# Optimization experiments

Measured on AMD Instinct MI355X. Metric: run time of the kernel, lower is better.

The kernel has to match this reference:

```python
import jax, jax.numpy as jnp
import numpy as np

VOCAB_SIZE = 4096
D_EMBED = 256
BETA = 0.25  # unused: module returns raw commit_loss; beta applied by caller


def setup_inputs() -> dict:
    key = jax.random.key(0)
    k_h, k_e = jax.random.split(key)
    h = jax.random.normal(k_h, (16, D_EMBED, 32, 32), dtype=jnp.float32)
    embedding = jax.random.normal(k_e, (VOCAB_SIZE, D_EMBED), dtype=jnp.float32)
    return {"h": h, "embedding": embedding}


def reference(h, embedding):
    B, C, H, W = h.shape
    h = h.astype(jnp.float32)
    # (B, C, H, W) -> (N, C) with N = B*H*W
    h_flat = jnp.transpose(h, (0, 2, 3, 1)).reshape(-1, C)
    dist = (
        jnp.sum(h_flat * h_flat, axis=1, keepdims=True)
        + jnp.sum(embedding * embedding, axis=1)
        - 2.0 * jnp.einsum("nc,vc->nv", h_flat, embedding)
    )
    indices_flat = jnp.argmin(dist, axis=1)
    indices = indices_flat.reshape(B, H, W)
    # gather codebook vectors and restore (B, C, H, W)
    z_q = jnp.transpose(embedding[indices_flat].reshape(B, H, W, C), (0, 3, 1, 2))
    commit_loss = jnp.mean((h - jax.lax.stop_gradient(z_q)) ** 2)
    # straight-through estimator
    z_q_st = h + jax.lax.stop_gradient(z_q - h)
    return z_q_st, indices, commit_loss
```

## Files before the change

### kernel.cpp

```cpp
#include <hip/hip_runtime.h>

#define D 256
#define VOCAB 4096
#define NTOT 16384
#define N_OUT0 4194304

typedef _Float16 half8 __attribute__((ext_vector_type(8)));
typedef float f32x4 __attribute__((ext_vector_type(4)));
typedef unsigned long long u64;

__device__ __forceinline__ u64 pack_key(float d, int v) {
    unsigned u = __float_as_uint(d);
    u ^= ((unsigned)((int)u >> 31)) | 0x80000000u;
    return ((u64)u << 32) | (unsigned)v;
}

__device__ __forceinline__ float unpack_dist(u64 k) {
    unsigned u = (unsigned)(k >> 32);
    u = (u & 0x80000000u) ? (u ^ 0x80000000u) : ~u;
    return __uint_as_float(u);
}

__global__ __launch_bounds__(256) void k_pack(const float* __restrict__ h,
                                              const float* __restrict__ emb,
                                              _Float16* __restrict__ Apk,
                                              _Float16* __restrict__ Bpk,
                                              float* __restrict__ hsqp,
                                              float* __restrict__ ht,
                                              float* __restrict__ esq,
                                              float* __restrict__ e2maxp,
                                              float* __restrict__ out2) {
    __shared__ float S[8192];
    const int tid = threadIdx.x;
    const int bid = blockIdx.x;
    if (bid < 512) {
        const int bm = bid >> 3, w = bid & 7;
        const int b = bm >> 2, p0 = (bm & 3) * 256;
        const float* src = h + ((size_t)b << 18) + p0;
#pragma unroll 4
        for (int cl = 0; cl < 32; ++cl)
            S[cl * 256 + tid] = src[(size_t)(w * 32 + cl) << 10 | (unsigned)tid];
        __syncthreads();
        float sq = 0.0f;
#pragma unroll
        for (int cl = 0; cl < 32; ++cl) {
            float t = S[cl * 256 + tid];
            sq = fmaf(t, t, sq);
        }
        hsqp[(size_t)(bm * 8 + w) * 256 + tid] = sq;
        float* htr = ht + ((size_t)(bm * 256 + tid)) * D + w * 32;
#pragma unroll
        for (int c4 = 0; c4 < 8; ++c4) {
            float4 t;
            t.x = S[(c4 * 4 + 0) * 256 + tid];
            t.y = S[(c4 * 4 + 1) * 256 + tid];
            t.z = S[(c4 * 4 + 2) * 256 + tid];
            t.w = S[(c4 * 4 + 3) * 256 + tid];
            *(float4*)(htr + c4 * 4) = t;
        }
        _Float16* dstT = Apk + (size_t)bm * 65536 + (size_t)w * 8192;
#pragma unroll
        for (int i = 0; i < 4; ++i) {
            alignas(16) _Float16 hi[8];
#pragma unroll
            for (int j = 0; j < 8; ++j) hi[j] = (_Float16)S[(i * 8 + j) * 256 + tid];
            *(half8*)(dstT + i * 2048 + tid * 8) = *(half8*)hi;
        }
    } else if (bid < 768) {
        const int bid2 = bid - 512;
        const int bn = bid2 >> 3, w = bid2 & 7;
        const int v0 = bn * 128;
#pragma unroll 4
        for (int i = 0; i < 16; ++i) {
            int flat = i * 256 + tid;
            int r = flat >> 5, cl = flat & 31;
            S[cl * 129 + r] = emb[(size_t)(v0 + r) * D + w * 32 + cl];
        }
        __syncthreads();
        _Float16* dstT = Bpk + (size_t)bn * 32768 + (size_t)w * 4096;
#pragma unroll
        for (int i = 0; i < 2; ++i) {
            int s = i * 256 + tid;
            int q = s >> 7, r = s & 127;
            alignas(16) _Float16 hi[8];
#pragma unroll
            for (int j = 0; j < 8; ++j) hi[j] = (_Float16)S[(q * 8 + j) * 129 + r];
            *(half8*)(dstT + q * 1024 + r * 8) = *(half8*)hi;
        }
    } else {
        __shared__ float sm[4];
        const int pid = bid - 768;
        const int lane = tid & 63, wv = tid >> 6;
        const int v0 = pid * 64;
        float lmax = 0.0f;
#pragma unroll 4
        for (int i = 0; i < 16; ++i) {
            int v = v0 + i * 4 + wv;
            float4 e = *(const float4*)(emb + (size_t)v * D + lane * 4);
            float s = e.x * e.x + e.y * e.y + e.z * e.z + e.w * e.w;
#pragma unroll
            for (int m = 32; m >= 1; m >>= 1) s += __shfl_xor(s, m, 64);
            if (lane == 0) esq[v] = s;
            lmax = fmaxf(lmax, s);
        }
        if (lane == 0) sm[wv] = lmax;
        __syncthreads();
        if (tid == 0) {
            e2maxp[pid] = fmaxf(fmaxf(sm[0], sm[1]), fmaxf(sm[2], sm[3]));
            if (pid == 0) out2[0] = 0.0f;
        }
    }
}

__global__ __launch_bounds__(256, 3) void k_gemm(const _Float16* __restrict__ Apk,
                                                 const _Float16* __restrict__ Bpk,
                                                 const float* __restrict__ esq,
                                                 u64* __restrict__ keys2) {
    __shared__ u64 t2[4096];

    const int tid = threadIdx.x;
    const int bid = blockIdx.x;
    const int swz = (bid & 7) * 512 + (bid >> 3);
    const int bm = swz >> 5, bn = swz & 31;
    const int m0 = bm * 128, n0 = bn * 128;

    const int wv = tid >> 6, l = tid & 63;
    const int wm = wv & 1, wn = wv >> 1;
    const int quad = l >> 4, j16 = l & 15;

    const _Float16* aP = Apk + (size_t)(bm >> 1) * 65536 + (size_t)(bm & 1) * 1024
                       + quad * 2048 + (wm * 64 + j16) * 8;
    const _Float16* bP = Bpk + (size_t)bn * 32768
                       + quad * 1024 + (wn * 64 + j16) * 8;

    f32x4 acc[4][4];
#pragma unroll
    for (int i = 0; i < 4; ++i)
#pragma unroll
        for (int j = 0; j < 4; ++j) acc[i][j] = (f32x4)0.0f;

    half8 af[4], bf[4], afn[4], bfn[4];
#pragma unroll
    for (int mt = 0; mt < 4; ++mt) af[mt] = *(const half8*)(aP + mt * 128);
#pragma unroll
    for (int nt = 0; nt < 4; ++nt) bf[nt] = *(const half8*)(bP + nt * 128);

#pragma unroll
    for (int w = 0; w < 8; ++w) {
        if (w < 7) {
#pragma unroll
            for (int mt = 0; mt < 4; ++mt)
                afn[mt] = *(const half8*)(aP + (w + 1) * 8192 + mt * 128);
#pragma unroll
            for (int nt = 0; nt < 4; ++nt)
                bfn[nt] = *(const half8*)(bP + (w + 1) * 4096 + nt * 128);
        }
        __builtin_amdgcn_s_setprio(1);
#pragma unroll
        for (int mt = 0; mt < 4; ++mt)
#pragma unroll
            for (int nt = 0; nt < 4; ++nt)
                acc[mt][nt] = __builtin_amdgcn_mfma_f32_16x16x32_f16(af[mt], bf[nt], acc[mt][nt], 0, 0, 0);
        __builtin_amdgcn_s_setprio(0);
#pragma unroll
        for (int mt = 0; mt < 4; ++mt) af[mt] = afn[mt];
#pragma unroll
        for (int nt = 0; nt < 4; ++nt) bf[nt] = bfn[nt];
    }

    float es[4];
    int vidx[4];
#pragma unroll
    for (int nt = 0; nt < 4; ++nt) {
        vidx[nt] = n0 + wn * 64 + nt * 16 + j16;
        es[nt] = esq[vidx[nt]];
    }

    u64 M1 = ~0ULL, M2 = ~0ULL;
#pragma unroll
    for (int pass = 0; pass < 2; ++pass) {
        if (wn == pass) {
#pragma unroll
            for (int mt = 0; mt < 4; ++mt) {
#pragma unroll
                for (int r = 0; r < 4; ++r) {
                    float d1 = __builtin_inff(), d2 = __builtin_inff();
                    int i1 = 0, i2 = 0;
#pragma unroll
                    for (int nt = 0; nt < 4; ++nt) {
                        float dv = es[nt] - 2.0f * acc[mt][nt][r];
                        bool c1 = dv < d1;
                        bool c2 = dv < d2;
                        d2 = c1 ? d1 : (c2 ? dv : d2);
                        i2 = c1 ? i1 : (c2 ? vidx[nt] : i2);
                        d1 = c1 ? dv : d1;
                        i1 = c1 ? vidx[nt] : i1;
                    }
                    int row = wm * 64 + mt * 16 + quad * 4 + r;
                    u64* p = t2 + ((size_t)(row * 16 + (j16 ^ (row & 7))) * 2);
                    p[0] = pack_key(d1, i1);
                    p[1] = pack_key(d2, i2);
                }
            }
        }
        __syncthreads();
        if (tid < 128) {
            const int row = tid;
#pragma unroll
            for (int j = 0; j < 16; ++j) {
                const u64* p = t2 + ((size_t)(row * 16 + (j ^ (row & 7))) * 2);
                u64 a1 = p[0], a2 = p[1];
                u64 x = M1 > a1 ? M1 : a1;
                M1 = M1 < a1 ? M1 : a1;
                u64 y = M2 < a2 ? M2 : a2;
                M2 = x < y ? x : y;
            }
        }
        __syncthreads();
    }
    if (tid < 128) {
        keys2[(size_t)(m0 + tid) * 64 + bn * 2 + 0] = M1;
        keys2[(size_t)(m0 + tid) * 64 + bn * 2 + 1] = M2;
    }
}

__device__ __forceinline__ u64 exact_key_ht(const float* __restrict__ ht,
                                            const float* __restrict__ emb,
                                            const float* __restrict__ esq,
                                            int rg, int v, int lane) {
    const float4 h4 = *(const float4*)(ht + (size_t)rg * D + lane * 4);
    const float4 e4 = *(const float4*)(emb + (size_t)v * D + lane * 4);
    float p = h4.x * e4.x;
    p = fmaf(h4.y, e4.y, p);
    p = fmaf(h4.z, e4.z, p);
    p = fmaf(h4.w, e4.w, p);
#pragma unroll
    for (int m = 32; m >= 1; m >>= 1) p += __shfl_xor(p, m, 64);
    return pack_key(esq[v] - 2.0f * p, v);
}

__global__ __launch_bounds__(256) void k_refine(const float* __restrict__ ht,
                                                const float* __restrict__ emb,
                                                const float* __restrict__ esq,
                                                const float* __restrict__ hsqp,
                                                const float* __restrict__ e2maxp,
                                                const u64* __restrict__ keys2,
                                                float* __restrict__ out1) {
    __shared__ float sE2;
    const int tid = threadIdx.x;
    const int lane = tid & 63;
    const int w = tid >> 6;
    const int n0 = blockIdx.x * 32;

    if (tid < 64) {
        float m = e2maxp[tid];
#pragma unroll
        for (int s = 32; s >= 1; s >>= 1) m = fmaxf(m, __shfl_xor(m, s, 64));
        if (tid == 0) sE2 = m;
    }
    __syncthreads();
    const float e2m = sE2;

    int rg = n0 + w * 8;
    u64 key = keys2[(size_t)rg * 64 + lane];
#pragma unroll 1
    for (int rr = 0; rr < 8; ++rr, ++rg) {
        u64 keyn = 0;
        if (rr < 7) keyn = keys2[(size_t)(rg + 1) * 64 + lane];
        u64 gm = key;
#pragma unroll
        for (int m = 32; m >= 1; m >>= 1) {
            u64 o = __shfl_xor(gm, m, 64);
            gm = o < gm ? o : gm;
        }
        float hq = 0.0f;
#pragma unroll
        for (int k = 0; k < 8; ++k) hq += hsqp[(size_t)(rg >> 8) * 2048 + k * 256 + (rg & 255)];
        const float thr = unpack_dist(gm) + 4.0e-3f * sqrtf(hq * e2m) + 1e-2f;
        u64 cmask = __ballot(unpack_dist(key) <= thr);
        u64 bestk;
        if (__popcll(cmask) == 1) {
            bestk = gm;
        } else {
            bestk = ~0ULL;
            u64 rescan = 0;
            u64 cm = cmask;
            while (cm) {
                int L = __ffsll((long long)cm) - 1;
                cm &= cm - 1;
                if (L & 1) {
                    rescan |= 1ull << (L >> 1);
                } else {
                    u64 kL = __shfl(key, L, 64);
                    u64 ek = exact_key_ht(ht, emb, esq, rg, (int)(kL & 0xFFFFFFFFu), lane);
                    bestk = ek < bestk ? ek : bestk;
                }
            }
            while (rescan) {
                int bnr = __ffsll((long long)rescan) - 1;
                rescan &= rescan - 1;
                const float* htr = ht + (size_t)rg * D;
                u64 k0 = ~0ULL, k1 = ~0ULL;
#pragma unroll
                for (int c = 0; c < 2; ++c) {
                    int v = bnr * 128 + c * 64 + lane;
                    float p = 0.0f;
#pragma unroll 8
                    for (int d = 0; d < D; d += 4) {
                        float4 hh = *(const float4*)(htr + d);
                        float4 ee = *(const float4*)(emb + (size_t)v * D + d);
                        p = fmaf(hh.x, ee.x, p);
                        p = fmaf(hh.y, ee.y, p);
                        p = fmaf(hh.z, ee.z, p);
                        p = fmaf(hh.w, ee.w, p);
                    }
                    u64 kc = pack_key(esq[v] - 2.0f * p, v);
                    if (c == 0) k0 = kc; else k1 = kc;
                }
                u64 m1 = k0 < k1 ? k0 : k1, m2 = k0 < k1 ? k1 : k0;
#pragma unroll
                for (int m = 32; m >= 1; m >>= 1) {
                    u64 o1 = __shfl_xor(m1, m, 64), o2 = __shfl_xor(m2, m, 64);
                    u64 hi = m1 > o1 ? m1 : o1;
                    m1 = m1 < o1 ? m1 : o1;
                    u64 lo2 = m2 < o2 ? m2 : o2;
                    m2 = hi < lo2 ? hi : lo2;
                }
                u64 e1 = exact_key_ht(ht, emb, esq, rg, (int)(m1 & 0xFFFFFFFFu), lane);
                u64 e2 = exact_key_ht(ht, emb, esq, rg, (int)(m2 & 0xFFFFFFFFu), lane);
                bestk = e1 < bestk ? e1 : bestk;
                bestk = e2 < bestk ? e2 : bestk;
            }
        }
        if (lane == 0) out1[rg] = (float)(int)(bestk & 0xFFFFFFFFu);
        key = keyn;
    }
}

__global__ __launch_bounds__(256) void k_out(const float* __restrict__ h,
                                             const float* __restrict__ emb,
                                             const float* __restrict__ out1,
                                             float* __restrict__ out0,
                                             float* __restrict__ out2) {
    __shared__ float zq[32][260];
    __shared__ float wred[4];
    const int tid = threadIdx.x;
    const int lane = tid & 63;
    const int w = tid >> 6;
    const int n0 = blockIdx.x * 32;
    const int b = n0 >> 10;
    const int p0 = n0 & 1023;
#pragma unroll
    for (int rr = 0; rr < 8; ++rr) {
        int r = w * 8 + rr;
        unsigned idx = (unsigned)(int)out1[n0 + r];
        float4 e4 = *(const float4*)(emb + (size_t)idx * D + lane * 4);
        *(float4*)&zq[r][lane * 4] = e4;
    }
    __syncthreads();
    float lsum = 0.0f;
    const size_t base = ((size_t)b * D) << 10;
#pragma unroll 4
    for (int it = 0; it < 32; ++it) {
        int c = it * 8 + (tid >> 5);
        int pp = tid & 31;
        float z = zq[pp][c];
        size_t g = base + ((size_t)c << 10) + p0 + pp;
        float hv = h[g];
        out0[g] = hv + (z - hv);
        float d = hv - z;
        lsum = fmaf(d, d, lsum);
    }
#pragma unroll
    for (int m = 32; m >= 1; m >>= 1) lsum += __shfl_xor(lsum, m, 64);
    if (lane == 0) wred[w] = lsum;
    __syncthreads();
    if (tid == 0)
        atomicAdd(out2, (wred[0] + wred[1] + wred[2] + wred[3]) * (1.0f / (float)N_OUT0));
}

extern "C" void kernel_launch(void* const* d_in, const int* in_sizes, int n_in,
                              void* d_out, int out_size, void* d_ws, size_t ws_size,
                              hipStream_t stream) {
    const float* h = (const float*)d_in[0];
    const float* emb = (const float*)d_in[1];
    float* out0 = (float*)d_out;
    float* out1 = out0 + N_OUT0;
    float* out2 = out1 + NTOT;

    char* wsb = (char*)d_ws;
    _Float16* Apk = (_Float16*)wsb;
    _Float16* Bpk = (_Float16*)(wsb + 8388608);
    float* esq = (float*)(wsb + 10485760);
    float* hsqp = (float*)(wsb + 10502144);
    float* e2maxp = (float*)(wsb + 11026432);
    u64* keys2 = (u64*)(wsb + 11028480);

    hipLaunchKernelGGL(k_pack, dim3(832), dim3(256), 0, stream, h, emb, Apk, Bpk, hsqp, out0, esq, e2maxp, out2);
    hipLaunchKernelGGL(k_gemm, dim3(4096), dim3(256), 0, stream, Apk, Bpk, esq, keys2);
    hipLaunchKernelGGL(k_refine, dim3(NTOT / 32), dim3(256), 0, stream, out0, emb, esq, hsqp, e2maxp, keys2, out1);
    hipLaunchKernelGGL(k_out, dim3(NTOT / 32), dim3(256), 0, stream, h, emb, out1, out0, out2);
}
```

Before: 181.3 us.

## Pack codebook index into float low mantissa bits for top-2 candidate keys

Replaces 64-bit (distance,index) keys in the GEMM epilogue with 32-bit floats whose low 7 mantissa bits carry the local codebook index. The top-2 selection then uses fminf/fmaxf instead of 64-bit compares and selects, and the LDS scratch and global key buffer shrink by half. The refine kernel recovers full indices from the lane position plus the embedded bits. Because this truncates distance precision, the candidate threshold is widened (1e-2 to 5e-2) to keep the exact rescoring correct, which may send more rows down the slower rescan path.

```diff
diff --git a/kernel.cpp b/kernel.cpp
--- a/kernel.cpp
+++ b/kernel.cpp
@@ -13,12 +13,6 @@
     unsigned u = __float_as_uint(d);
     u ^= ((unsigned)((int)u >> 31)) | 0x80000000u;
     return ((u64)u << 32) | (unsigned)v;
-}
-
-__device__ __forceinline__ float unpack_dist(u64 k) {
-    unsigned u = (unsigned)(k >> 32);
-    u = (u & 0x80000000u) ? (u ^ 0x80000000u) : ~u;
-    return __uint_as_float(u);
 }
 
 __global__ __launch_bounds__(256) void k_pack(const float* __restrict__ h,
@@ -115,8 +109,8 @@
 __global__ __launch_bounds__(256, 3) void k_gemm(const _Float16* __restrict__ Apk,
                                                  const _Float16* __restrict__ Bpk,
                                                  const float* __restrict__ esq,
-                                                 u64* __restrict__ keys2) {
-    __shared__ u64 t2[4096];
+                                                 float2* __restrict__ keys2) {
+    __shared__ float2 t2[2048];
 
     const int tid = threadIdx.x;
     const int bid = blockIdx.x;
@@ -169,14 +163,14 @@
     }
 
     float es[4];
-    int vidx[4];
+    unsigned code[4];
 #pragma unroll
     for (int nt = 0; nt < 4; ++nt) {
-        vidx[nt] = n0 + wn * 64 + nt * 16 + j16;
-        es[nt] = esq[vidx[nt]];
-    }
-
-    u64 M1 = ~0ULL, M2 = ~0ULL;
+        code[nt] = (unsigned)(wn * 64 + nt * 16 + j16);
+        es[nt] = esq[n0 + (int)code[nt]];
+    }
+
+    float M1 = __builtin_inff(), M2 = __builtin_inff();
 #pragma unroll
     for (int pass = 0; pass < 2; ++pass) {
         if (wn == pass) {
@@ -184,22 +178,18 @@
             for (int mt = 0; mt < 4; ++mt) {
 #pragma unroll
                 for (int r = 0; r < 4; ++r) {
-                    float d1 = __builtin_inff(), d2 = __builtin_inff();
-                    int i1 = 0, i2 = 0;
+                    float c[4];
 #pragma unroll
                     for (int nt = 0; nt < 4; ++nt) {
                         float dv = es[nt] - 2.0f * acc[mt][nt][r];
-                        bool c1 = dv < d1;
-                        bool c2 = dv < d2;
-                        d2 = c1 ? d1 : (c2 ? dv : d2);
-                        i2 = c1 ? i1 : (c2 ? vidx[nt] : i2);
-                        d1 = c1 ? dv : d1;
-                        i1 = c1 ? vidx[nt] : i1;
+                        c[nt] = __uint_as_float((__float_as_uint(dv) & ~127u) | code[nt]);
                     }
+                    float p = fminf(c[0], c[1]), q = fmaxf(c[0], c[1]);
+                    float rr = fminf(c[2], c[3]), s = fmaxf(c[2], c[3]);
+                    float m1 = fminf(p, rr);
+                    float m2 = fminf(fmaxf(p, rr), fminf(q, s));
                     int row = wm * 64 + mt * 16 + quad * 4 + r;
-                    u64* p = t2 + ((size_t)(row * 16 + (j16 ^ (row & 7))) * 2);
-                    p[0] = pack_key(d1, i1);
-                    p[1] = pack_key(d2, i2);
+                    t2[row * 16 + (j16 ^ (row & 7))] = make_float2(m1, m2);
                 }
             }
         }
@@ -208,20 +198,16 @@
             const int row = tid;
 #pragma unroll
             for (int j = 0; j < 16; ++j) {
-                const u64* p = t2 + ((size_t)(row * 16 + (j ^ (row & 7))) * 2);
-                u64 a1 = p[0], a2 = p[1];
-                u64 x = M1 > a1 ? M1 : a1;
-                M1 = M1 < a1 ? M1 : a1;
-                u64 y = M2 < a2 ? M2 : a2;
-                M2 = x < y ? x : y;
+                float2 a = t2[row * 16 + (j ^ (row & 7))];
+                float t = fmaxf(M1, a.x);
+                M1 = fminf(M1, a.x);
+                M2 = fminf(fminf(M2, a.y), t);
             }
         }
         __syncthreads();
     }
-    if (tid < 128) {
-        keys2[(size_t)(m0 + tid) * 64 + bn * 2 + 0] = M1;
-        keys2[(size_t)(m0 + tid) * 64 + bn * 2 + 1] = M2;
-    }
+    if (tid < 128)
+        keys2[(size_t)(m0 + tid) * 32 + bn] = make_float2(M1, M2);
 }
 
 __device__ __forceinline__ u64 exact_key_ht(const float* __restrict__ ht,
@@ -244,7 +230,7 @@
                                                 const float* __restrict__ esq,
                                                 const float* __restrict__ hsqp,
                                                 const float* __restrict__ e2maxp,
-                                                const u64* __restrict__ keys2,
+                                                const float* __restrict__ keys2f,
                                                 float* __restrict__ out1) {
     __shared__ float sE2;
     const int tid = threadIdx.x;
@@ -262,27 +248,26 @@
     const float e2m = sE2;
 
     int rg = n0 + w * 8;
-    u64 key = keys2[(size_t)rg * 64 + lane];
+    float key = keys2f[(size_t)rg * 64 + lane];
 #pragma unroll 1
     for (int rr = 0; rr < 8; ++rr, ++rg) {
-        u64 keyn = 0;
-        if (rr < 7) keyn = keys2[(size_t)(rg + 1) * 64 + lane];
-        u64 gm = key;
-#pragma unroll
-        for (int m = 32; m >= 1; m >>= 1) {
-            u64 o = __shfl_xor(gm, m, 64);
-            gm = o < gm ? o : gm;
-        }
+        float keyn = 0.0f;
+        if (rr < 7) keyn = keys2f[(size_t)(rg + 1) * 64 + lane];
+        float gm = key;
+#pragma unroll
+        for (int m = 32; m >= 1; m >>= 1) gm = fminf(gm, __shfl_xor(gm, m, 64));
         float hq = 0.0f;
 #pragma unroll
         for (int k = 0; k < 8; ++k) hq += hsqp[(size_t)(rg >> 8) * 2048 + k * 256 + (rg & 255)];
-        const float thr = unpack_dist(gm) + 4.0e-3f * sqrtf(hq * e2m) + 1e-2f;
-        u64 cmask = __ballot(unpack_dist(key) <= thr);
-        u64 bestk;
+        const float thr = gm + 4.0e-3f * sqrtf(hq * e2m) + 5.0e-2f;
+        u64 cmask = __ballot(key <= thr);
+        int bidx;
         if (__popcll(cmask) == 1) {
-            bestk = gm;
+            u64 own = __ballot(key == gm);
+            int L = __ffsll((long long)own) - 1;
+            bidx = (L >> 1) * 128 + (int)(__float_as_uint(gm) & 127u);
         } else {
-            bestk = ~0ULL;
+            u64 bestk = ~0ULL;
             u64 rescan = 0;
             u64 cm = cmask;
             while (cm) {
@@ -291,8 +276,9 @@
                 if (L & 1) {
                     rescan |= 1ull << (L >> 1);
                 } else {
-                    u64 kL = __shfl(key, L, 64);
-                    u64 ek = exact_key_ht(ht, emb, esq, rg, (int)(kL & 0xFFFFFFFFu), lane);
+                    float kL = __shfl(key, L, 64);
+                    int v = (L >> 1) * 128 + (int)(__float_as_uint(kL) & 127u);
+                    u64 ek = exact_key_ht(ht, emb, esq, rg, v, lane);
                     bestk = ek < bestk ? ek : bestk;
                 }
             }
@@ -331,8 +317,9 @@
                 bestk = e1 < bestk ? e1 : bestk;
                 bestk = e2 < bestk ? e2 : bestk;
             }
-        }
-        if (lane == 0) out1[rg] = (float)(int)(bestk & 0xFFFFFFFFu);
+            bidx = (int)(bestk & 0xFFFFFFFFu);
+        }
+        if (lane == 0) out1[rg] = (float)bidx;
         key = keyn;
     }
 }
@@ -394,10 +381,10 @@
     float* esq = (float*)(wsb + 10485760);
     float* hsqp = (float*)(wsb + 10502144);
     float* e2maxp = (float*)(wsb + 11026432);
-    u64* keys2 = (u64*)(wsb + 11028480);
+    float* keys2f = (float*)(wsb + 11028480);
 
     hipLaunchKernelGGL(k_pack, dim3(832), dim3(256), 0, stream, h, emb, Apk, Bpk, hsqp, out0, esq, e2maxp, out2);
-    hipLaunchKernelGGL(k_gemm, dim3(4096), dim3(256), 0, stream, Apk, Bpk, esq, keys2);
-    hipLaunchKernelGGL(k_refine, dim3(NTOT / 32), dim3(256), 0, stream, out0, emb, esq, hsqp, e2maxp, keys2, out1);
+    hipLaunchKernelGGL(k_gemm, dim3(4096), dim3(256), 0, stream, Apk, Bpk, esq, (float2*)keys2f);
+    hipLaunchKernelGGL(k_refine, dim3(NTOT / 32), dim3(256), 0, stream, out0, emb, esq, hsqp, e2maxp, keys2f, out1);
     hipLaunchKernelGGL(k_out, dim3(NTOT / 32), dim3(256), 0, stream, h, emb, out1, out0, out2);
 }
```

Result: faster. 170.3 us (-6.1%).
